# Kernel tuning notes

Hardware: AMD Instinct MI355X
Metric: run time of the kernel (lower is better)

Reference implementation:

```python
import jax, jax.numpy as jnp
import numpy as np

B, L, WIN = 65536, 240, 24
EMB_SZS = [(367, 20), (7, 4), (24, 8)]
N_CONT = 16
H1, H2, OUT_SZ = 512, 256, 24
N_EMB = sum(nf for _, nf in EMB_SZS)
NUM_WAVE = 6 * (WIN // 2) + 6 * (WIN // 4)  # 108


def pool_matrix(lin, w):
    # PyTorch AdaptiveAvgPool1d: bin i averages x[floor(i*lin/w) : ceil((i+1)*lin/w)]
    P = np.zeros((lin, w), np.float32)
    for i in range(w):
        s = (i * lin) // w
        e = -((-(i + 1) * lin) // w)
        P[s:e, i] = 1.0 / (e - s)
    return jnp.asarray(P)


def conv1(x, w, dil):
    # single-channel 1D cross-correlation, no bias; x: [B, Lin], w: [ks]
    ks = w.shape[0]
    lout = x.shape[-1] - dil * (ks - 1)
    return sum(w[k] * x[:, k * dil:k * dil + lout] for k in range(ks))


def branch(xw, wa, wb):
    # conv(ks, dil=1) -> adaptive_avg_pool(12) -> leaky_relu(0.1), then same with dil=2 -> pool(6)
    ca = conv1(xw, wa, 1)                                   # [B, L-ks+1]
    fa = jax.nn.leaky_relu(ca @ pool_matrix(ca.shape[-1], WIN // 2), 0.1)  # [B,12]
    cb = conv1(fa, wb, 2)                                   # [B, 12-2*(ks-1)]
    fb = jax.nn.leaky_relu(cb @ pool_matrix(cb.shape[-1], WIN // 4), 0.1)  # [B,6]
    return fa, fb


def setup_inputs() -> dict:
    key = jax.random.key(0)
    ks_list = list(range(1, 7))
    keys = jax.random.split(key, 32)
    d = {}
    d['x_window'] = jax.random.normal(keys[0], (B, 1, L), jnp.float32)
    cats = [jax.random.randint(jax.random.fold_in(keys[1], i), (B,), 0, ni)
            for i, (ni, _) in enumerate(EMB_SZS)]
    d['x_cat'] = jnp.stack(cats, axis=1).astype(jnp.int64)
    d['x_cont'] = jax.random.normal(keys[2], (B, N_CONT), jnp.float32)
    for i, ks in enumerate(ks_list):
        d[f'wk{ks}a'] = jax.random.normal(keys[3 + 2 * i], (ks,), jnp.float32) * 0.5
        d[f'wk{ks}b'] = jax.random.normal(keys[4 + 2 * i], (ks,), jnp.float32) * 0.5
    for i, (ni, nf) in enumerate(EMB_SZS):
        d[f'E{i}'] = jax.random.normal(keys[16 + i], (ni, nf), jnp.float32) * 0.01
    d['bn_g'] = jnp.ones((N_CONT,), jnp.float32)
    d['bn_b'] = jnp.zeros((N_CONT,), jnp.float32)
    n_in = N_EMB + N_CONT
    d['W1'] = jax.random.normal(keys[20], (n_in, H1), jnp.float32) * (1.0 / np.sqrt(n_in))
    d['b1'] = jnp.zeros((H1,), jnp.float32)
    d['W2'] = jax.random.normal(keys[21], (H1, H2), jnp.float32) * (1.0 / np.sqrt(H1))
    d['b2'] = jnp.zeros((H2,), jnp.float32)
    d['Wlin'] = jax.random.normal(keys[22], (NUM_WAVE + H2, OUT_SZ), jnp.float32) * (1.0 / np.sqrt(NUM_WAVE + H2))
    return d


def reference(x_window, x_cat, x_cont,
              wk1a, wk1b, wk2a, wk2b, wk3a, wk3b, wk4a, wk4b, wk5a, wk5b, wk6a, wk6b,
              E0, E1, E2, bn_g, bn_b, W1, b1, W2, b2, Wlin):
    xw = x_window[:, 0, :]  # [B, L]
    feats = []
    for wa, wb in [(wk1a, wk1b), (wk2a, wk2b), (wk3a, wk3b),
                   (wk4a, wk4b), (wk5a, wk5b), (wk6a, wk6b)]:
        fa, fb = branch(xw, wa, wb)
        feats += [fa, fb]
    ffc = jnp.concatenate(feats, axis=1)  # [B, 108]
    # embeddings
    emb = jnp.concatenate([E0[x_cat[:, 0]], E1[x_cat[:, 1]], E2[x_cat[:, 2]]], axis=1)  # [B, 32]
    # BatchNorm1d on continuous features (training-mode batch stats, eps=1e-5)
    m = jnp.mean(x_cont, axis=0)
    v = jnp.var(x_cont, axis=0)
    xc = (x_cont - m) / jnp.sqrt(v + 1e-5) * bn_g + bn_b
    x = jnp.concatenate([emb, xc], axis=1)  # [B, 48]
    x = jax.nn.relu(x @ W1 + b1)
    x = jax.nn.relu(x @ W2 + b2)  # [B, 256]
    fc = jnp.concatenate([ffc, x], axis=1)  # [B, 364]
    return fc @ Wlin  # [B, 24]
```

## Files before the change

### kernel.cpp

```cpp
#include <hip/hip_runtime.h>

typedef __bf16 bf16x8 __attribute__((ext_vector_type(8)));
typedef float  f32x4  __attribute__((ext_vector_type(4)));
typedef unsigned short ushort_t;

#define B_TOTAL 65536

__device__ __forceinline__ ushort_t f2bf(float f) {
  unsigned u = __builtin_bit_cast(unsigned, f);
  u += 0x7fffu + ((u >> 16) & 1u);
  return (ushort_t)(u >> 16);
}
__device__ __forceinline__ unsigned pk2(float lo, float hi) {
  unsigned r;
  asm("v_cvt_pk_bf16_f32 %0, %1, %2" : "=v"(r) : "v"(lo), "v"(hi));
  return r;
}
__device__ __forceinline__ float lrelu(float v) { return v >= 0.f ? v : 0.1f * v; }
__device__ __forceinline__ bf16x8 ld_frag(const ushort_t* p8) {
  return __builtin_bit_cast(bf16x8, *(const uint4*)p8);
}
__device__ __forceinline__ bf16x8 ld_tile(const ushort_t* base, int tile, int lane) {
  return __builtin_bit_cast(bf16x8,
      *(const uint4*)((const char*)base + tile * 1024 + lane * 16));
}
__device__ __forceinline__ char* frag_addr4(ushort_t* base, int k, int s15, int st) {
  int kb = k >> 5, g = (k >> 3) & 3, i = k & 7;
  return (char*)base + (((kb * 4 + st) * 64) + s15 + g * 16) * 16 + i * 2;
}
__device__ __forceinline__ f32x4 mfma16(bf16x8 a, bf16x8 b, f32x4 c) {
  return __builtin_amdgcn_mfma_f32_16x16x32_bf16(a, b, c, 0, 0, 0);
}

__global__ __launch_bounds__(256) void bn_partial(const float* __restrict__ xc,
                                                  float* __restrict__ ws) {
  __shared__ float red[512];
  const int t = threadIdx.x;
  const int c = t & 15, g = t >> 4;
  const int r0 = blockIdx.x * 256;
  float s = 0.f, q = 0.f;
  for (int i = 0; i < 16; ++i) {
    float v = xc[(size_t)(r0 + g + i * 16) * 16 + c];
    s += v; q += v * v;
  }
  red[t] = s; red[256 + t] = q;
  __syncthreads();
  if (t < 16) {
    float ss = 0.f, qq = 0.f;
    for (int gg = 0; gg < 16; ++gg) { ss += red[gg * 16 + t]; qq += red[256 + gg * 16 + t]; }
    ws[blockIdx.x * 32 + t] = ss;
    ws[blockIdx.x * 32 + 16 + t] = qq;
  }
}

__global__ __launch_bounds__(256) void bn_final(const float* __restrict__ ws_in,
                                                float* __restrict__ ws_out,
                                                const float* __restrict__ g_,
                                                const float* __restrict__ b_) {
  __shared__ float red[512];
  const int t = threadIdx.x;
  const int c = t & 15, g = t >> 4;
  float s = 0.f, q = 0.f;
  for (int i = 0; i < 16; ++i) {
    int blk = g * 16 + i;
    s += ws_in[blk * 32 + c];
    q += ws_in[blk * 32 + 16 + c];
  }
  red[t] = s; red[256 + t] = q;
  __syncthreads();
  if (t < 16) {
    float ss = 0.f, qq = 0.f;
    for (int gg = 0; gg < 16; ++gg) { ss += red[gg * 16 + t]; qq += red[256 + gg * 16 + t]; }
    float mean  = ss / (float)B_TOTAL;
    float var   = qq / (float)B_TOTAL - mean * mean;
    float scale = g_[t] / sqrtf(var + 1e-5f);
    ws_out[8192 + t]      = scale;
    ws_out[8192 + 16 + t] = b_[t] - mean * scale;
  }
}

__global__ __launch_bounds__(256) void pack_weights(const float* __restrict__ W1,
                                                    const float* __restrict__ W2,
                                                    const float* __restrict__ Wl,
                                                    ushort_t* __restrict__ w1p,
                                                    ushort_t* __restrict__ w2p,
                                                    ushort_t* __restrict__ wlp) {
  int u = blockIdx.x * 256 + threadIdx.x;
  if (u < 32768) {
    int i = u & 7, lane = (u >> 3) & 63, kb = u >> 14;
    int k = kb * 32 + ((lane >> 4) << 3) + i;
    int n = (((u >> 9) & 31) << 4) + (lane & 15);
    w1p[u] = f2bf(k < 48 ? W1[k * 512 + n] : 0.f);
  } else if (u < 32768 + 131072) {
    int v = u - 32768;
    int i = v & 7, lane = (v >> 3) & 63, kb = v >> 13;
    int k = kb * 32 + ((lane >> 4) << 3) + i;
    int n = (((v >> 9) & 15) << 4) + (lane & 15);
    w2p[v] = f2bf(W2[k * 256 + n]);
  } else if (u < 32768 + 131072 + 12288) {
    int v = u - (32768 + 131072);
    int i = v & 7, lane = (v >> 3) & 63, kb = v >> 10;
    int k = kb * 32 + ((lane >> 4) << 3) + i;
    int n = (((v >> 9) & 1) << 4) + (lane & 15);
    float val = 0.f;
    if (n < 24) {
      if (k < 108)       val = Wl[k * 24 + n];
      else if (k >= 128) val = Wl[(k - 20) * 24 + n];
    }
    wlp[v] = f2bf(val);
  }
}

struct WkPtrs { const float* wk[12]; };

__global__ __launch_bounds__(256) void pack_conv(WkPtrs wp,
                                                 ushort_t* __restrict__ Apack,
                                                 ushort_t* __restrict__ Bpack) {
  int u = blockIdx.x * 256 + threadIdx.x;
  if (u < 20480) {
    int i = u & 7, lane = (u >> 3) & 63;
    int knt = u >> 9;
    int kb = knt / 5, nt = knt % 5;
    int k = kb * 32 + ((lane >> 4) << 3) + i;
    int n = nt * 16 + (lane & 15);
    float val = 0.f;
    if (n < 72 && k < 240) {
      int br = n / 12, ii = n - br * 12, ks = br + 1, lin = 240 - br;
      int si = ii * lin / 12, ei = ((ii + 1) * lin + 11) / 12;
      const float* wa = wp.wk[2 * br];
      float acc = 0.f;
      for (int kk = 0; kk < ks; ++kk) {
        int j = k - kk;
        if (j >= si && j < ei) acc += wa[kk];
      }
      val = acc / (float)(ei - si);
    }
    Apack[u] = f2bf(val);
  } else if (u < 20480 + 6144) {
    int v = u - 20480;
    int i = v & 7, lane = (v >> 3) & 63;
    int knt = v >> 9;
    int kb = knt / 3, nt = knt % 3;
    int kcol = kb * 32 + ((lane >> 4) << 3) + i;
    int n = nt * 16 + (lane & 15);
    float val = 0.f;
    if (n < 36 && kcol < 108) {
      int brk = kcol / 18, ii = kcol - brk * 18;
      int brn = n / 6, j = n - brn * 6;
      if (brk == brn && ii < 12) {
        int ks = brn + 1, lcb = 12 - 2 * brn;
        int sj = j * lcb / 6, ej = ((j + 1) * lcb + 5) / 6;
        const float* wb = wp.wk[2 * brn + 1];
        float acc = 0.f;
        for (int kk = 0; kk < ks; ++kk) {
          int q = ii - 2 * kk;
          if (q >= sj && q < ej) acc += wb[kk];
        }
        val = acc / (float)(ej - sj);
      }
    }
    Bpack[v] = f2bf(val);
  }
}

struct FusedParams {
  const float* xw;
  const int*   xcat;
  const float* xcont;
  const float* E0; const float* E1; const float* E2;
  const float* b1; const float* b2;
  const ushort_t* Apack; const ushort_t* Bpack;
  const ushort_t* w1p; const ushort_t* w2p; const ushort_t* wlp;
  const float* stats;
  float*       out;
};

__global__ __launch_bounds__(1024, 8) void fused_kernel(FusedParams p) {
  __shared__ __align__(16) char smem[57344];
  ushort_t* s_xw  = (ushort_t*)smem;
  ushort_t* s_h1  = (ushort_t*)smem;
  ushort_t* s_h2  = (ushort_t*)smem;
  ushort_t* s_cf  = (ushort_t*)(smem + 32768);
  ushort_t* s_x48 = (ushort_t*)(smem + 49152);

  const int t    = threadIdx.x;
  const int lane = t & 63;
  const int w    = t >> 6;
  const int quad = lane >> 4;
  const int s15  = lane & 15;
  const int s0   = blockIdx.x * 64;
  const f32x4 fzero = {0.f, 0.f, 0.f, 0.f};

  ((uint4*)s_cf)[t] = uint4{0, 0, 0, 0};
  if (t < 128) {
    *(uint4*)((char*)s_xw + (28 + (t >> 5)) * 1024 + 512 + (t & 31) * 16) = uint4{0, 0, 0, 0};
  } else if (t < 256) {
    int tt = t - 128;
    *(uint4*)((char*)s_x48 + (4 + (tt >> 5)) * 1024 + 512 + (tt & 31) * 16) = uint4{0, 0, 0, 0};
  }
  for (int u = t; u < 64 * 60; u += 1024) {
    int s = u / 60, m4 = u - s * 60;
    float4 v = *(const float4*)(p.xw + (size_t)(s0 + s) * 240 + 4 * m4);
    uint2 pkv; pkv.x = pk2(v.x, v.y); pkv.y = pk2(v.z, v.w);
    int tile = (m4 >> 3) * 4 + (s >> 4);
    *(uint2*)((char*)s_xw + (tile * 64 + (s & 15) + ((m4 >> 1) & 3) * 16) * 16
              + (m4 & 1) * 8) = pkv;
  }
  for (int u = t; u < 64 * 48; u += 1024) {
    int s = u / 48, c = u - s * 48, gs = s0 + s;
    float v;
    if (c < 20)      v = p.E0[(size_t)p.xcat[gs * 3 + 0] * 20 + c];
    else if (c < 24) v = p.E1[(size_t)p.xcat[gs * 3 + 1] * 4 + (c - 20)];
    else if (c < 32) v = p.E2[(size_t)p.xcat[gs * 3 + 2] * 8 + (c - 24)];
    else { int cc = c - 32; v = p.xcont[(size_t)gs * 16 + cc] * p.stats[cc] + p.stats[16 + cc]; }
    *(ushort_t*)frag_addr4(s_x48, c, s & 15, s >> 4) = f2bf(v);
  }
  __syncthreads();

  auto do0a = [&](int nt, int st) {
    f32x4 acc = fzero;
    #pragma unroll
    for (int kb = 0; kb < 8; ++kb) {
      bf16x8 a = ld_frag(p.Apack + (size_t)((kb * 5 + nt) * 64 + lane) * 8);
      bf16x8 b = ld_tile(s_xw, kb * 4 + st, lane);
      acc = mfma16(a, b, acc);
    }
    int n0 = nt * 16 + quad * 4;
    int br = n0 / 12;
    int col0 = n0 + 6 * br;
    *(unsigned*)frag_addr4(s_cf, col0, s15, st)     = pk2(lrelu(acc[0]), lrelu(acc[1]));
    *(unsigned*)frag_addr4(s_cf, col0 + 2, s15, st) = pk2(lrelu(acc[2]), lrelu(acc[3]));
  };
  do0a(w % 5, w / 5);
  if (w < 4) do0a((w + 16) % 5, (w + 16) / 5);
  __syncthreads();

  const int nt2 = w;
  uint4 pa[2];
  pa[0] = *(const uint4*)(p.w2p + (size_t)((0 * 16 + nt2) * 64 + lane) * 8);
  pa[1] = *(const uint4*)(p.w2p + (size_t)((1 * 16 + nt2) * 64 + lane) * 8);

  const int ntB = w % 3, stB = w / 3;
  f32x4 accB = fzero;
  if (w < 12) {
    #pragma unroll
    for (int kb = 0; kb < 4; ++kb) {
      bf16x8 a = ld_frag(p.Bpack + (size_t)((kb * 3 + ntB) * 64 + lane) * 8);
      bf16x8 b = ld_tile(s_cf, kb * 4 + stB, lane);
      accB = mfma16(a, b, accB);
    }
  }

  auto gemm1_half = [&](int h) {
    int gnt = h * 16 + w;
    bf16x8 a0 = ld_frag(p.w1p + (size_t)((0 * 32 + gnt) * 64 + lane) * 8);
    bf16x8 a1 = ld_frag(p.w1p + (size_t)((32 + gnt) * 64 + lane) * 8);
    f32x4 acc[4];
    #pragma unroll
    for (int st = 0; st < 4; ++st) {
      bf16x8 b0 = ld_tile(s_x48, 0 * 4 + st, lane);
      bf16x8 b1 = ld_tile(s_x48, 1 * 4 + st, lane);
      acc[st] = mfma16(a0, b0, fzero);
      acc[st] = mfma16(a1, b1, acc[st]);
    }
    int n0l = w * 16 + quad * 4;
    float4 bb = *(const float4*)(p.b1 + h * 256 + n0l);
    int kb1 = w >> 1;
    int g   = (w * 2 + (quad >> 1)) & 3;
    #pragma unroll
    for (int st = 0; st < 4; ++st) {
      float v0 = fmaxf(acc[st][0] + bb.x, 0.f);
      float v1 = fmaxf(acc[st][1] + bb.y, 0.f);
      float v2 = fmaxf(acc[st][2] + bb.z, 0.f);
      float v3 = fmaxf(acc[st][3] + bb.w, 0.f);
      uint2 pkv; pkv.x = pk2(v0, v1); pkv.y = pk2(v2, v3);
      *(uint2*)((char*)s_h1 + ((kb1 * 4 + st) * 64 + s15 + g * 16) * 16
                + (quad & 1) * 8) = pkv;
    }
  };
  gemm1_half(0);
  __syncthreads();

  if (w < 12) {
    int n0 = ntB * 16 + quad * 4;
    if (n0 < 36) {
      int br0 = n0 / 6, c0 = n0 + 12 * (br0 + 1);
      int n2 = n0 + 2, br2 = n2 / 6, c2 = n2 + 12 * (br2 + 1);
      *(unsigned*)frag_addr4(s_cf, c0, s15, stB) = pk2(lrelu(accB[0]), lrelu(accB[1]));
      *(unsigned*)frag_addr4(s_cf, c2, s15, stB) = pk2(lrelu(accB[2]), lrelu(accB[3]));
    }
  }

  f32x4 acc2[4];
  #pragma unroll
  for (int st = 0; st < 4; ++st) acc2[st] = fzero;

  auto gemm2_half = [&](int k0) {
    #pragma unroll
    for (int kk = 0; kk < 8; ++kk) {
      int kb = k0 + kk;
      bf16x8 a0 = __builtin_bit_cast(bf16x8, pa[kb & 1]);
      if (kb + 2 < 16) {
        pa[kb & 1] = *(const uint4*)(p.w2p + (size_t)(((kb + 2) * 16 + nt2) * 64 + lane) * 8);
      }
      #pragma unroll
      for (int st = 0; st < 4; ++st) {
        bf16x8 b = ld_tile(s_h1, kk * 4 + st, lane);
        acc2[st] = mfma16(a0, b, acc2[st]);
      }
    }
  };
  gemm2_half(0);
  __syncthreads();

  gemm1_half(1);
  __syncthreads();

  gemm2_half(8);
  __syncthreads();

  {
    int n0 = nt2 * 16 + quad * 4;
    float4 bb = *(const float4*)(p.b2 + n0);
    int kbh = nt2 >> 1;
    int g   = (nt2 * 2 + (quad >> 1)) & 3;
    #pragma unroll
    for (int st = 0; st < 4; ++st) {
      float v0 = fmaxf(acc2[st][0] + bb.x, 0.f);
      float v1 = fmaxf(acc2[st][1] + bb.y, 0.f);
      float v2 = fmaxf(acc2[st][2] + bb.z, 0.f);
      float v3 = fmaxf(acc2[st][3] + bb.w, 0.f);
      uint2 pkv; pkv.x = pk2(v0, v1); pkv.y = pk2(v2, v3);
      *(uint2*)((char*)s_h2 + ((kbh * 4 + st) * 64 + s15 + g * 16) * 16
                + (quad & 1) * 8) = pkv;
    }
  }
  __syncthreads();

  if (w < 8) {
    const int st = w & 3, nt = w >> 2;
    f32x4 acc = fzero;
    #pragma unroll
    for (int kb = 0; kb < 12; ++kb) {
      bf16x8 a = ld_frag(p.wlp + (size_t)((kb * 2 + nt) * 64 + lane) * 8);
      bf16x8 b = (kb < 4) ? ld_tile(s_cf, kb * 4 + st, lane)
                          : ld_tile(s_h2, (kb - 4) * 4 + st, lane);
      acc = mfma16(a, b, acc);
    }
    int n0 = nt * 16 + quad * 4;
    if (n0 < 24) {
      int sg = s0 + st * 16 + s15;
      *(float2*)(p.out + (size_t)sg * 24 + n0)     = make_float2(acc[0], acc[1]);
      *(float2*)(p.out + (size_t)sg * 24 + n0 + 2) = make_float2(acc[2], acc[3]);
    }
  }
}

extern "C" void kernel_launch(void* const* d_in, const int* in_sizes, int n_in,
                              void* d_out, int out_size, void* d_ws, size_t ws_size,
                              hipStream_t stream) {
  const float* xcont = (const float*)d_in[2];
  float* ws  = (float*)d_ws;
  char*  wsb = (char*)d_ws;
  ushort_t* w1p   = (ushort_t*)(wsb + 36864);
  ushort_t* w2p   = (ushort_t*)(wsb + 102400);
  ushort_t* wlp   = (ushort_t*)(wsb + 364544);
  ushort_t* Apack = (ushort_t*)(wsb + 389120);
  ushort_t* Bpack = (ushort_t*)(wsb + 430080);

  WkPtrs wp;
  for (int i = 0; i < 12; ++i) wp.wk[i] = (const float*)d_in[3 + i];
  pack_conv<<<104, 256, 0, stream>>>(wp, Apack, Bpack);
  bn_partial<<<256, 256, 0, stream>>>(xcont, ws);
  bn_final<<<1, 256, 0, stream>>>(ws, ws, (const float*)d_in[18], (const float*)d_in[19]);
  pack_weights<<<688, 256, 0, stream>>>((const float*)d_in[20], (const float*)d_in[22],
                                        (const float*)d_in[24], w1p, w2p, wlp);

  FusedParams p;
  p.xw    = (const float*)d_in[0];
  p.xcat  = (const int*)d_in[1];
  p.xcont = xcont;
  p.E0 = (const float*)d_in[15]; p.E1 = (const float*)d_in[16]; p.E2 = (const float*)d_in[17];
  p.b1 = (const float*)d_in[21]; p.b2 = (const float*)d_in[23];
  p.Apack = Apack; p.Bpack = Bpack;
  p.w1p = w1p; p.w2p = w2p; p.wlp = wlp;
  p.stats = ws + 8192;
  p.out = (float*)d_out;
  fused_kernel<<<B_TOTAL / 64, 1024, 0, stream>>>(p);
}
```

Baseline: 62.49 us.

## Merge prep kernels into one launch, finalize BN in fused kernel, retile GEMM2

The four setup kernels (conv packing, BN partial sums, BN final, weight packing) become a single prep launch with block-range dispatch. The BN finalize step moves into each block of the fused kernel, which reduces the 256 partial sums in shared memory. GEMM2 is retiled so each wave covers 2 N-tiles by 2 sample tiles instead of 1 by 4, and its weight prefetch is reissued after gemm1_half(1). This cuts launch overhead and reuses B fragments, but every fused block now redundantly re-reduces the BN partials.

```diff
diff --git a/kernel.cpp b/kernel.cpp
--- a/kernel.cpp
+++ b/kernel.cpp
@@ -32,134 +32,104 @@
   return __builtin_amdgcn_mfma_f32_16x16x32_bf16(a, b, c, 0, 0, 0);
 }
 
-__global__ __launch_bounds__(256) void bn_partial(const float* __restrict__ xc,
-                                                  float* __restrict__ ws) {
+struct PrepParams {
+  const float* W1; const float* W2; const float* Wl;
+  ushort_t* w1p; ushort_t* w2p; ushort_t* wlp;
+  ushort_t* Apack; ushort_t* Bpack;
+  const float* xc; float* ws;
+  const float* wk[12];
+};
+
+__global__ __launch_bounds__(256) void prep_all(PrepParams q) {
   __shared__ float red[512];
-  const int t = threadIdx.x;
-  const int c = t & 15, g = t >> 4;
-  const int r0 = blockIdx.x * 256;
-  float s = 0.f, q = 0.f;
-  for (int i = 0; i < 16; ++i) {
-    float v = xc[(size_t)(r0 + g + i * 16) * 16 + c];
-    s += v; q += v * v;
-  }
-  red[t] = s; red[256 + t] = q;
-  __syncthreads();
-  if (t < 16) {
-    float ss = 0.f, qq = 0.f;
-    for (int gg = 0; gg < 16; ++gg) { ss += red[gg * 16 + t]; qq += red[256 + gg * 16 + t]; }
-    ws[blockIdx.x * 32 + t] = ss;
-    ws[blockIdx.x * 32 + 16 + t] = qq;
-  }
-}
-
-__global__ __launch_bounds__(256) void bn_final(const float* __restrict__ ws_in,
-                                                float* __restrict__ ws_out,
-                                                const float* __restrict__ g_,
-                                                const float* __restrict__ b_) {
-  __shared__ float red[512];
-  const int t = threadIdx.x;
-  const int c = t & 15, g = t >> 4;
-  float s = 0.f, q = 0.f;
-  for (int i = 0; i < 16; ++i) {
-    int blk = g * 16 + i;
-    s += ws_in[blk * 32 + c];
-    q += ws_in[blk * 32 + 16 + c];
-  }
-  red[t] = s; red[256 + t] = q;
-  __syncthreads();
-  if (t < 16) {
-    float ss = 0.f, qq = 0.f;
-    for (int gg = 0; gg < 16; ++gg) { ss += red[gg * 16 + t]; qq += red[256 + gg * 16 + t]; }
-    float mean  = ss / (float)B_TOTAL;
-    float var   = qq / (float)B_TOTAL - mean * mean;
-    float scale = g_[t] / sqrtf(var + 1e-5f);
-    ws_out[8192 + t]      = scale;
-    ws_out[8192 + 16 + t] = b_[t] - mean * scale;
-  }
-}
-
-__global__ __launch_bounds__(256) void pack_weights(const float* __restrict__ W1,
-                                                    const float* __restrict__ W2,
-                                                    const float* __restrict__ Wl,
-                                                    ushort_t* __restrict__ w1p,
-                                                    ushort_t* __restrict__ w2p,
-                                                    ushort_t* __restrict__ wlp) {
-  int u = blockIdx.x * 256 + threadIdx.x;
-  if (u < 32768) {
-    int i = u & 7, lane = (u >> 3) & 63, kb = u >> 14;
-    int k = kb * 32 + ((lane >> 4) << 3) + i;
-    int n = (((u >> 9) & 31) << 4) + (lane & 15);
-    w1p[u] = f2bf(k < 48 ? W1[k * 512 + n] : 0.f);
-  } else if (u < 32768 + 131072) {
-    int v = u - 32768;
-    int i = v & 7, lane = (v >> 3) & 63, kb = v >> 13;
-    int k = kb * 32 + ((lane >> 4) << 3) + i;
-    int n = (((v >> 9) & 15) << 4) + (lane & 15);
-    w2p[v] = f2bf(W2[k * 256 + n]);
-  } else if (u < 32768 + 131072 + 12288) {
-    int v = u - (32768 + 131072);
-    int i = v & 7, lane = (v >> 3) & 63, kb = v >> 10;
-    int k = kb * 32 + ((lane >> 4) << 3) + i;
-    int n = (((v >> 9) & 1) << 4) + (lane & 15);
-    float val = 0.f;
-    if (n < 24) {
-      if (k < 108)       val = Wl[k * 24 + n];
-      else if (k >= 128) val = Wl[(k - 20) * 24 + n];
-    }
-    wlp[v] = f2bf(val);
-  }
-}
-
-struct WkPtrs { const float* wk[12]; };
-
-__global__ __launch_bounds__(256) void pack_conv(WkPtrs wp,
-                                                 ushort_t* __restrict__ Apack,
-                                                 ushort_t* __restrict__ Bpack) {
-  int u = blockIdx.x * 256 + threadIdx.x;
-  if (u < 20480) {
-    int i = u & 7, lane = (u >> 3) & 63;
-    int knt = u >> 9;
-    int kb = knt / 5, nt = knt % 5;
-    int k = kb * 32 + ((lane >> 4) << 3) + i;
-    int n = nt * 16 + (lane & 15);
-    float val = 0.f;
-    if (n < 72 && k < 240) {
-      int br = n / 12, ii = n - br * 12, ks = br + 1, lin = 240 - br;
-      int si = ii * lin / 12, ei = ((ii + 1) * lin + 11) / 12;
-      const float* wa = wp.wk[2 * br];
-      float acc = 0.f;
-      for (int kk = 0; kk < ks; ++kk) {
-        int j = k - kk;
-        if (j >= si && j < ei) acc += wa[kk];
-      }
-      val = acc / (float)(ei - si);
-    }
-    Apack[u] = f2bf(val);
-  } else if (u < 20480 + 6144) {
-    int v = u - 20480;
-    int i = v & 7, lane = (v >> 3) & 63;
-    int knt = v >> 9;
-    int kb = knt / 3, nt = knt % 3;
-    int kcol = kb * 32 + ((lane >> 4) << 3) + i;
-    int n = nt * 16 + (lane & 15);
-    float val = 0.f;
-    if (n < 36 && kcol < 108) {
-      int brk = kcol / 18, ii = kcol - brk * 18;
-      int brn = n / 6, j = n - brn * 6;
-      if (brk == brn && ii < 12) {
-        int ks = brn + 1, lcb = 12 - 2 * brn;
-        int sj = j * lcb / 6, ej = ((j + 1) * lcb + 5) / 6;
-        const float* wb = wp.wk[2 * brn + 1];
+  const int b = blockIdx.x, t = threadIdx.x;
+  if (b < 688) {
+    int u = b * 256 + t;
+    if (u < 32768) {
+      int i = u & 7, lane = (u >> 3) & 63, kb = u >> 14;
+      int k = kb * 32 + ((lane >> 4) << 3) + i;
+      int n = (((u >> 9) & 31) << 4) + (lane & 15);
+      q.w1p[u] = f2bf(k < 48 ? q.W1[k * 512 + n] : 0.f);
+    } else if (u < 32768 + 131072) {
+      int v = u - 32768;
+      int i = v & 7, lane = (v >> 3) & 63, kb = v >> 13;
+      int k = kb * 32 + ((lane >> 4) << 3) + i;
+      int n = (((v >> 9) & 15) << 4) + (lane & 15);
+      q.w2p[v] = f2bf(q.W2[k * 256 + n]);
+    } else {
+      int v = u - (32768 + 131072);
+      int i = v & 7, lane = (v >> 3) & 63, kb = v >> 10;
+      int k = kb * 32 + ((lane >> 4) << 3) + i;
+      int n = (((v >> 9) & 1) << 4) + (lane & 15);
+      float val = 0.f;
+      if (n < 24) {
+        if (k < 108)       val = q.Wl[k * 24 + n];
+        else if (k >= 128) val = q.Wl[(k - 20) * 24 + n];
+      }
+      q.wlp[v] = f2bf(val);
+    }
+  } else if (b < 792) {
+    int u = (b - 688) * 256 + t;
+    if (u < 20480) {
+      int i = u & 7, lane = (u >> 3) & 63;
+      int knt = u >> 9;
+      int kb = knt / 5, nt = knt % 5;
+      int k = kb * 32 + ((lane >> 4) << 3) + i;
+      int n = nt * 16 + (lane & 15);
+      float val = 0.f;
+      if (n < 72 && k < 240) {
+        int br = n / 12, ii = n - br * 12, ks = br + 1, lin = 240 - br;
+        int si = ii * lin / 12, ei = ((ii + 1) * lin + 11) / 12;
+        const float* wa = q.wk[2 * br];
         float acc = 0.f;
         for (int kk = 0; kk < ks; ++kk) {
-          int q = ii - 2 * kk;
-          if (q >= sj && q < ej) acc += wb[kk];
+          int j = k - kk;
+          if (j >= si && j < ei) acc += wa[kk];
         }
-        val = acc / (float)(ej - sj);
-      }
-    }
-    Bpack[v] = f2bf(val);
+        val = acc / (float)(ei - si);
+      }
+      q.Apack[u] = f2bf(val);
+    } else {
+      int v = u - 20480;
+      int i = v & 7, lane = (v >> 3) & 63;
+      int knt = v >> 9;
+      int kb = knt / 3, nt = knt % 3;
+      int kcol = kb * 32 + ((lane >> 4) << 3) + i;
+      int n = nt * 16 + (lane & 15);
+      float val = 0.f;
+      if (n < 36 && kcol < 108) {
+        int brk = kcol / 18, ii = kcol - brk * 18;
+        int brn = n / 6, j = n - brn * 6;
+        if (brk == brn && ii < 12) {
+          int ks = brn + 1, lcb = 12 - 2 * brn;
+          int sj = j * lcb / 6, ej = ((j + 1) * lcb + 5) / 6;
+          const float* wb = q.wk[2 * brn + 1];
+          float acc = 0.f;
+          for (int kk = 0; kk < ks; ++kk) {
+            int qq = ii - 2 * kk;
+            if (qq >= sj && qq < ej) acc += wb[kk];
+          }
+          val = acc / (float)(ej - sj);
+        }
+      }
+      q.Bpack[v] = f2bf(val);
+    }
+  } else {
+    const int c = t & 15, g = t >> 4;
+    const int r0 = (b - 792) * 256;
+    float s = 0.f, qq = 0.f;
+    for (int i = 0; i < 16; ++i) {
+      float v = q.xc[(size_t)(r0 + g + i * 16) * 16 + c];
+      s += v; qq += v * v;
+    }
+    red[t] = s; red[256 + t] = qq;
+    __syncthreads();
+    if (t < 16) {
+      float ss = 0.f, sq = 0.f;
+      for (int gg = 0; gg < 16; ++gg) { ss += red[gg * 16 + t]; sq += red[256 + gg * 16 + t]; }
+      q.ws[(b - 792) * 32 + t] = ss;
+      q.ws[(b - 792) * 32 + 16 + t] = sq;
+    }
   }
 }
 
@@ -171,17 +141,19 @@
   const float* b1; const float* b2;
   const ushort_t* Apack; const ushort_t* Bpack;
   const ushort_t* w1p; const ushort_t* w2p; const ushort_t* wlp;
-  const float* stats;
+  const float* bnws;
+  const float* bn_g; const float* bn_b;
   float*       out;
 };
 
 __global__ __launch_bounds__(1024, 8) void fused_kernel(FusedParams p) {
-  __shared__ __align__(16) char smem[57344];
+  __shared__ __align__(16) char smem[57472];
   ushort_t* s_xw  = (ushort_t*)smem;
   ushort_t* s_h1  = (ushort_t*)smem;
   ushort_t* s_h2  = (ushort_t*)smem;
   ushort_t* s_cf  = (ushort_t*)(smem + 32768);
   ushort_t* s_x48 = (ushort_t*)(smem + 49152);
+  float*    s_bn  = (float*)(smem + 57344);
 
   const int t    = threadIdx.x;
   const int lane = t & 63;
@@ -191,13 +163,6 @@
   const int s0   = blockIdx.x * 64;
   const f32x4 fzero = {0.f, 0.f, 0.f, 0.f};
 
-  ((uint4*)s_cf)[t] = uint4{0, 0, 0, 0};
-  if (t < 128) {
-    *(uint4*)((char*)s_xw + (28 + (t >> 5)) * 1024 + 512 + (t & 31) * 16) = uint4{0, 0, 0, 0};
-  } else if (t < 256) {
-    int tt = t - 128;
-    *(uint4*)((char*)s_x48 + (4 + (tt >> 5)) * 1024 + 512 + (tt & 31) * 16) = uint4{0, 0, 0, 0};
-  }
   for (int u = t; u < 64 * 60; u += 1024) {
     int s = u / 60, m4 = u - s * 60;
     float4 v = *(const float4*)(p.xw + (size_t)(s0 + s) * 240 + 4 * m4);
@@ -206,13 +171,39 @@
     *(uint2*)((char*)s_xw + (tile * 64 + (s & 15) + ((m4 >> 1) & 3) * 16) * 16
               + (m4 & 1) * 8) = pkv;
   }
+  float* redbuf = (float*)s_x48;
+  if (t < 512) {
+    int c = t & 31, g16 = t >> 5;
+    float acc = 0.f;
+    for (int i = 0; i < 16; ++i) acc += p.bnws[(g16 * 16 + i) * 32 + c];
+    redbuf[g16 * 32 + c] = acc;
+  }
+  ((uint4*)s_cf)[t] = uint4{0, 0, 0, 0};
+  if (t >= 512 && t < 640) {
+    int tt = t - 512;
+    *(uint4*)((char*)s_xw + (28 + (tt >> 5)) * 1024 + 512 + (tt & 31) * 16) = uint4{0, 0, 0, 0};
+  }
+  __syncthreads();
+  if (t < 16) {
+    float ss = 0.f, sq = 0.f;
+    for (int g = 0; g < 16; ++g) { ss += redbuf[g * 32 + t]; sq += redbuf[g * 32 + 16 + t]; }
+    float mean  = ss / (float)B_TOTAL;
+    float var   = sq / (float)B_TOTAL - mean * mean;
+    float scale = p.bn_g[t] / sqrtf(var + 1e-5f);
+    s_bn[t]      = scale;
+    s_bn[16 + t] = p.bn_b[t] - mean * scale;
+  }
+  __syncthreads();
+  if (t < 128) {
+    *(uint4*)((char*)s_x48 + (4 + (t >> 5)) * 1024 + 512 + (t & 31) * 16) = uint4{0, 0, 0, 0};
+  }
   for (int u = t; u < 64 * 48; u += 1024) {
     int s = u / 48, c = u - s * 48, gs = s0 + s;
     float v;
     if (c < 20)      v = p.E0[(size_t)p.xcat[gs * 3 + 0] * 20 + c];
     else if (c < 24) v = p.E1[(size_t)p.xcat[gs * 3 + 1] * 4 + (c - 20)];
     else if (c < 32) v = p.E2[(size_t)p.xcat[gs * 3 + 2] * 8 + (c - 24)];
-    else { int cc = c - 32; v = p.xcont[(size_t)gs * 16 + cc] * p.stats[cc] + p.stats[16 + cc]; }
+    else { int cc = c - 32; v = p.xcont[(size_t)gs * 16 + cc] * s_bn[cc] + s_bn[16 + cc]; }
     *(ushort_t*)frag_addr4(s_x48, c, s & 15, s >> 4) = f2bf(v);
   }
   __syncthreads();
@@ -235,10 +226,8 @@
   if (w < 4) do0a((w + 16) % 5, (w + 16) / 5);
   __syncthreads();
 
-  const int nt2 = w;
-  uint4 pa[2];
-  pa[0] = *(const uint4*)(p.w2p + (size_t)((0 * 16 + nt2) * 64 + lane) * 8);
-  pa[1] = *(const uint4*)(p.w2p + (size_t)((1 * 16 + nt2) * 64 + lane) * 8);
+  const int np = w >> 1;
+  const int sh = w & 1;
 
   const int ntB = w % 3, stB = w / 3;
   f32x4 accB = fzero;
@@ -255,30 +244,32 @@
     int gnt = h * 16 + w;
     bf16x8 a0 = ld_frag(p.w1p + (size_t)((0 * 32 + gnt) * 64 + lane) * 8);
     bf16x8 a1 = ld_frag(p.w1p + (size_t)((32 + gnt) * 64 + lane) * 8);
-    f32x4 acc[4];
-    #pragma unroll
-    for (int st = 0; st < 4; ++st) {
-      bf16x8 b0 = ld_tile(s_x48, 0 * 4 + st, lane);
-      bf16x8 b1 = ld_tile(s_x48, 1 * 4 + st, lane);
-      acc[st] = mfma16(a0, b0, fzero);
-      acc[st] = mfma16(a1, b1, acc[st]);
-    }
     int n0l = w * 16 + quad * 4;
     float4 bb = *(const float4*)(p.b1 + h * 256 + n0l);
     int kb1 = w >> 1;
     int g   = (w * 2 + (quad >> 1)) & 3;
     #pragma unroll
     for (int st = 0; st < 4; ++st) {
-      float v0 = fmaxf(acc[st][0] + bb.x, 0.f);
-      float v1 = fmaxf(acc[st][1] + bb.y, 0.f);
-      float v2 = fmaxf(acc[st][2] + bb.z, 0.f);
-      float v3 = fmaxf(acc[st][3] + bb.w, 0.f);
+      bf16x8 b0 = ld_tile(s_x48, st, lane);
+      bf16x8 b1 = ld_tile(s_x48, 4 + st, lane);
+      f32x4 acc = mfma16(a0, b0, fzero);
+      acc = mfma16(a1, b1, acc);
+      float v0 = fmaxf(acc[0] + bb.x, 0.f);
+      float v1 = fmaxf(acc[1] + bb.y, 0.f);
+      float v2 = fmaxf(acc[2] + bb.z, 0.f);
+      float v3 = fmaxf(acc[3] + bb.w, 0.f);
       uint2 pkv; pkv.x = pk2(v0, v1); pkv.y = pk2(v2, v3);
       *(uint2*)((char*)s_h1 + ((kb1 * 4 + st) * 64 + s15 + g * 16) * 16
                 + (quad & 1) * 8) = pkv;
     }
   };
   gemm1_half(0);
+
+  uint4 pa[2][2];
+  pa[0][0] = *(const uint4*)(p.w2p + (size_t)((0 * 16 + 2 * np + 0) * 64 + lane) * 8);
+  pa[0][1] = *(const uint4*)(p.w2p + (size_t)((0 * 16 + 2 * np + 1) * 64 + lane) * 8);
+  pa[1][0] = *(const uint4*)(p.w2p + (size_t)((1 * 16 + 2 * np + 0) * 64 + lane) * 8);
+  pa[1][1] = *(const uint4*)(p.w2p + (size_t)((1 * 16 + 2 * np + 1) * 64 + lane) * 8);
   __syncthreads();
 
   if (w < 12) {
@@ -291,22 +282,25 @@
     }
   }
 
-  f32x4 acc2[4];
+  f32x4 acc2[2][2];
   #pragma unroll
-  for (int st = 0; st < 4; ++st) acc2[st] = fzero;
+  for (int jm = 0; jm < 2; ++jm) { acc2[jm][0] = fzero; acc2[jm][1] = fzero; }
 
   auto gemm2_half = [&](int k0) {
     #pragma unroll
     for (int kk = 0; kk < 8; ++kk) {
       int kb = k0 + kk;
-      bf16x8 a0 = __builtin_bit_cast(bf16x8, pa[kb & 1]);
-      if (kb + 2 < 16) {
-        pa[kb & 1] = *(const uint4*)(p.w2p + (size_t)(((kb + 2) * 16 + nt2) * 64 + lane) * 8);
+      bf16x8 a0 = __builtin_bit_cast(bf16x8, pa[kb & 1][0]);
+      bf16x8 a1 = __builtin_bit_cast(bf16x8, pa[kb & 1][1]);
+      if (kk < 6) {
+        pa[kb & 1][0] = *(const uint4*)(p.w2p + (size_t)(((kb + 2) * 16 + 2 * np + 0) * 64 + lane) * 8);
+        pa[kb & 1][1] = *(const uint4*)(p.w2p + (size_t)(((kb + 2) * 16 + 2 * np + 1) * 64 + lane) * 8);
       }
       #pragma unroll
-      for (int st = 0; st < 4; ++st) {
-        bf16x8 b = ld_tile(s_h1, kk * 4 + st, lane);
-        acc2[st] = mfma16(a0, b, acc2[st]);
+      for (int sl = 0; sl < 2; ++sl) {
+        bf16x8 b = ld_tile(s_h1, kk * 4 + 2 * sh + sl, lane);
+        acc2[0][sl] = mfma16(a0, b, acc2[0][sl]);
+        acc2[1][sl] = mfma16(a1, b, acc2[1][sl]);
       }
     }
   };
@@ -314,22 +308,29 @@
   __syncthreads();
 
   gemm1_half(1);
+  pa[0][0] = *(const uint4*)(p.w2p + (size_t)((8 * 16 + 2 * np + 0) * 64 + lane) * 8);
+  pa[0][1] = *(const uint4*)(p.w2p + (size_t)((8 * 16 + 2 * np + 1) * 64 + lane) * 8);
+  pa[1][0] = *(const uint4*)(p.w2p + (size_t)((9 * 16 + 2 * np + 0) * 64 + lane) * 8);
+  pa[1][1] = *(const uint4*)(p.w2p + (size_t)((9 * 16 + 2 * np + 1) * 64 + lane) * 8);
   __syncthreads();
 
   gemm2_half(8);
   __syncthreads();
 
-  {
-    int n0 = nt2 * 16 + quad * 4;
+  #pragma unroll
+  for (int jm = 0; jm < 2; ++jm) {
+    int nt = 2 * np + jm;
+    int n0 = nt * 16 + quad * 4;
     float4 bb = *(const float4*)(p.b2 + n0);
-    int kbh = nt2 >> 1;
-    int g   = (nt2 * 2 + (quad >> 1)) & 3;
-    #pragma unroll
-    for (int st = 0; st < 4; ++st) {
-      float v0 = fmaxf(acc2[st][0] + bb.x, 0.f);
-      float v1 = fmaxf(acc2[st][1] + bb.y, 0.f);
-      float v2 = fmaxf(acc2[st][2] + bb.z, 0.f);
-      float v3 = fmaxf(acc2[st][3] + bb.w, 0.f);
+    int kbh = nt >> 1;
+    int g   = (nt * 2 + (quad >> 1)) & 3;
+    #pragma unroll
+    for (int sl = 0; sl < 2; ++sl) {
+      int st = 2 * sh + sl;
+      float v0 = fmaxf(acc2[jm][sl][0] + bb.x, 0.f);
+      float v1 = fmaxf(acc2[jm][sl][1] + bb.y, 0.f);
+      float v2 = fmaxf(acc2[jm][sl][2] + bb.z, 0.f);
+      float v3 = fmaxf(acc2[jm][sl][3] + bb.w, 0.f);
       uint2 pkv; pkv.x = pk2(v0, v1); pkv.y = pk2(v2, v3);
       *(uint2*)((char*)s_h2 + ((kbh * 4 + st) * 64 + s15 + g * 16) * 16
                 + (quad & 1) * 8) = pkv;
@@ -368,13 +369,13 @@
   ushort_t* Apack = (ushort_t*)(wsb + 389120);
   ushort_t* Bpack = (ushort_t*)(wsb + 430080);
 
-  WkPtrs wp;
-  for (int i = 0; i < 12; ++i) wp.wk[i] = (const float*)d_in[3 + i];
-  pack_conv<<<104, 256, 0, stream>>>(wp, Apack, Bpack);
-  bn_partial<<<256, 256, 0, stream>>>(xcont, ws);
-  bn_final<<<1, 256, 0, stream>>>(ws, ws, (const float*)d_in[18], (const float*)d_in[19]);
-  pack_weights<<<688, 256, 0, stream>>>((const float*)d_in[20], (const float*)d_in[22],
-                                        (const float*)d_in[24], w1p, w2p, wlp);
+  PrepParams q;
+  q.W1 = (const float*)d_in[20]; q.W2 = (const float*)d_in[22]; q.Wl = (const float*)d_in[24];
+  q.w1p = w1p; q.w2p = w2p; q.wlp = wlp;
+  q.Apack = Apack; q.Bpack = Bpack;
+  q.xc = xcont; q.ws = ws;
+  for (int i = 0; i < 12; ++i) q.wk[i] = (const float*)d_in[3 + i];
+  prep_all<<<1048, 256, 0, stream>>>(q);
 
   FusedParams p;
   p.xw    = (const float*)d_in[0];
@@ -384,7 +385,8 @@
   p.b1 = (const float*)d_in[21]; p.b2 = (const float*)d_in[23];
   p.Apack = Apack; p.Bpack = Bpack;
   p.w1p = w1p; p.w2p = w2p; p.wlp = wlp;
-  p.stats = ws + 8192;
+  p.bnws = ws;
+  p.bn_g = (const float*)d_in[18]; p.bn_b = (const float*)d_in[19];
   p.out = (float*)d_out;
   fused_kernel<<<B_TOTAL / 64, 1024, 0, stream>>>(p);
 }
```

Measured after the change: 61.28 us. No clear change (-1.9%).
